# Performance work log

Measured on AMD Instinct MI355X. Metric: run time of the kernel, lower is better.

The kernel has to match this reference:

```python
import jax, jax.numpy as jnp
import numpy as np

NC = 80          # num classes
REG_MAX = 16     # DFL bins
STRIDES = (8, 16, 32)
FEAT_HW = ((80, 80), (40, 40), (20, 20))
MAX_DET = 100
CONF_THRES = 0.25
IOU_THRES = 0.45
PRE_TOPK = 1000  # pre-NMS candidate count (EfficientNMS-style preselection)


def setup_inputs() -> dict:
    key = jax.random.key(0)
    k1, k2, k3 = jax.random.split(key, 3)
    B = 32
    no = 4 * REG_MAX + NC  # 144
    return {
        "p3": jax.random.normal(k1, (B, no, 80, 80), dtype=jnp.float32),
        "p4": jax.random.normal(k2, (B, no, 40, 40), dtype=jnp.float32),
        "p5": jax.random.normal(k3, (B, no, 20, 20), dtype=jnp.float32),
    }


def _make_anchors():
    # grid_cell_offset = 0.5, matching ultralytics make_anchors
    pts, strs = [], []
    for (h, w), s in zip(FEAT_HW, STRIDES):
        sx = jnp.arange(w, dtype=jnp.float32) + 0.5
        sy = jnp.arange(h, dtype=jnp.float32) + 0.5
        yy, xx = jnp.meshgrid(sy, sx, indexing="ij")
        pts.append(jnp.stack([xx.ravel(), yy.ravel()], axis=-1))  # [h*w, 2]
        strs.append(jnp.full((h * w, 1), float(s), dtype=jnp.float32))
    return jnp.concatenate(pts, 0), jnp.concatenate(strs, 0)  # [A,2], [A,1]


def _pairwise_iou(b):
    # b: [K, 4] xyxy
    area = (b[:, 2] - b[:, 0]) * (b[:, 3] - b[:, 1])
    lt = jnp.maximum(b[:, None, :2], b[None, :, :2])
    rb = jnp.minimum(b[:, None, 2:], b[None, :, 2:])
    wh = jnp.clip(rb - lt, 0.0)
    inter = wh[..., 0] * wh[..., 1]
    return inter / (area[:, None] + area[None, :] - inter + 1e-7)


def _nms_single(bxyxy, conf):
    # Greedy class-agnostic NMS over PRE_TOPK score-sorted boxes.
    K = bxyxy.shape[0]
    iou = _pairwise_iou(bxyxy)  # [K, K]
    idx = jnp.arange(K)

    def step(suppressed, xs):
        i, row = xs
        keep = jnp.logical_and(jnp.logical_not(suppressed[i]), conf[i] > 0.0)
        suppressed = jnp.logical_or(suppressed, keep & (row > IOU_THRES) & (idx > i))
        return suppressed, keep

    _, keeps = jax.lax.scan(step, jnp.zeros(K, dtype=bool), (idx, iou))
    return keeps  # [K] bool


def reference(p3, p4, p5):
    feats = [p3, p4, p5]
    B = p3.shape[0]
    no = 4 * REG_MAX + NC
    # concat across scales: [B, no, A]
    x_cat = jnp.concatenate([f.reshape(B, no, -1) for f in feats], axis=2)
    box, cls = x_cat[:, : 4 * REG_MAX], x_cat[:, 4 * REG_MAX:]

    anchors, strd = _make_anchors()  # [A,2], [A,1]
    A = box.shape[-1]

    # DFL: softmax over reg_max bins, expectation with arange weights
    prob = jax.nn.softmax(box.reshape(B, 4, REG_MAX, A), axis=2)
    dist = jnp.einsum("bkra,r->bka", prob, jnp.arange(REG_MAX, dtype=jnp.float32))

    # dist2bbox (xywh) then scale by stride
    anc = anchors.T  # [2, A]
    lt, rb = dist[:, :2], dist[:, 2:]
    x1y1 = anc - lt
    x2y2 = anc + rb
    dbox = jnp.concatenate([(x1y1 + x2y2) * 0.5, x2y2 - x1y1], axis=1) * strd.T  # [B,4,A]

    boxes = dbox.transpose(0, 2, 1)                       # [B, A, 4] xywh
    scores = jax.nn.sigmoid(cls).transpose(0, 2, 1)       # [B, A, NC] (score_activation=1)

    # class-agnostic: best class per box
    conf = scores.max(-1)                                 # [B, A]
    cls_id = jnp.argmax(scores, -1)                       # [B, A]
    conf_m = jnp.where(conf > CONF_THRES, conf, -1.0)

    topv, topi = jax.lax.top_k(conf_m, PRE_TOPK)          # [B, K]
    bsel = jnp.take_along_axis(boxes, topi[..., None], axis=1)  # [B, K, 4]
    cx, cy, w, h = bsel[..., 0], bsel[..., 1], bsel[..., 2], bsel[..., 3]
    bxyxy = jnp.stack([cx - w * 0.5, cy - h * 0.5, cx + w * 0.5, cy + h * 0.5], -1)

    keeps = jax.vmap(_nms_single)(bxyxy, topv)            # [B, K]
    kept_scores = jnp.where(keeps, topv, -1.0)
    dv, di = jax.lax.top_k(kept_scores, MAX_DET)          # [B, MAX_DET]
    valid = dv > 0.0

    det_scores = jnp.where(valid, dv, 0.0)
    det_boxes = jnp.take_along_axis(bxyxy, di[..., None], axis=1) * valid[..., None]
    sel_cls = jnp.take_along_axis(jnp.take_along_axis(cls_id, topi, 1), di, 1)
    det_classes = jnp.where(valid, sel_cls, 0).astype(jnp.int32)
    num_dets = valid.sum(-1, keepdims=True).astype(jnp.int32)
    return num_dets, det_boxes, det_scores, det_classes
```

## Files before the change

kernel.cpp:

```cpp
#include <hip/hip_runtime.h>
#include <math.h>

#define NCLS 80
#define NA 8400
#define NB 32
#define NO 144
#define PRE_TOPK 1000
#define MAX_DET 100

template<int HW, int WDIM, int S>
__device__ __forceinline__ void decode_blk(
    const float* __restrict__ src, int b, int a0, int aoff,
    float* __restrict__ conf, int* __restrict__ clsid, float* __restrict__ box,
    float* s_tile)
{
    int t = threadIdx.x;
    int w = t >> 6;
    int l = t & 63;

    {
        int ch_base = w * 36;
        int chl = ch_base + (l >> 4);
        int aq = (l & 15) * 4;
        int aqc = a0 + aq; if (aqc > HW - 4) aqc = HW - 4;
        const float* gsrc = src + ((size_t)b * NO) * HW + aqc;
        float4 stg[9];
        #pragma unroll
        for (int i = 0; i < 9; ++i)
            stg[i] = *(const float4*)(gsrc + (size_t)(chl + i * 4) * HW);
        #pragma unroll
        for (int i = 0; i < 9; ++i)
            *(float4*)&s_tile[(chl + i * 4) * 64 + aq] = stg[i];
    }
    __syncthreads();

    float v[16];
    #pragma unroll
    for (int r = 0; r < 16; ++r) v[r] = s_tile[(w * 16 + r) * 64 + l];
    float mm = v[0];
    #pragma unroll
    for (int r = 1; r < 16; ++r) mm = fmaxf(mm, v[r]);
    float sum = 0.f, d = 0.f;
    #pragma unroll
    for (int r = 0; r < 16; ++r) {
        float e = __expf(v[r] - mm);
        sum += e;
        d += e * (float)r;
    }
    d *= 1.0f / sum;

    float c[20];
    #pragma unroll
    for (int cc = 0; cc < 20; ++cc) c[cc] = s_tile[(64 + w * 20 + cc) * 64 + l];
    float m = c[0]; int ii = 0;
    #pragma unroll
    for (int cc = 1; cc < 20; ++cc) if (c[cc] > m) { m = c[cc]; ii = cc; }

    __syncthreads();

    float* s_dfl = s_tile;
    float* s_mx  = s_tile + 320;
    int*   s_id  = (int*)(s_tile + 640);
    s_dfl[l * 5 + w] = d;
    s_mx[l * 5 + w]  = m;
    s_id[l * 5 + w]  = w * 20 + ii;
    __syncthreads();

    if (t < 64 && a0 + t < HW) {
        int pos2 = a0 + t;
        float d0 = s_dfl[t * 5 + 0], d1 = s_dfl[t * 5 + 1];
        float d2 = s_dfl[t * 5 + 2], d3 = s_dfl[t * 5 + 3];
        float bm = s_mx[t * 5 + 0]; int bid = s_id[t * 5 + 0];
        float m1 = s_mx[t * 5 + 1]; if (m1 > bm) { bm = m1; bid = s_id[t * 5 + 1]; }
        float m2 = s_mx[t * 5 + 2]; if (m2 > bm) { bm = m2; bid = s_id[t * 5 + 2]; }
        float m3 = s_mx[t * 5 + 3]; if (m3 > bm) { bm = m3; bid = s_id[t * 5 + 3]; }
        float conf_v = 1.0f / (1.0f + __expf(-bm));

        float ax = (float)(pos2 % WDIM) + 0.5f;
        float ay = (float)(pos2 / WDIM) + 0.5f;
        float x1 = ax - d0, y1 = ay - d1;
        float x2 = ax + d2, y2 = ay + d3;
        float cx = ((x1 + x2) * 0.5f) * (float)S;
        float cy = ((y1 + y2) * 0.5f) * (float)S;
        float ww = (x2 - x1) * (float)S;
        float hh = (y2 - y1) * (float)S;

        size_t gid = (size_t)b * NA + aoff + pos2;
        conf[gid]  = conf_v;
        clsid[gid] = bid;
        *(float4*)(box + gid * 4) = make_float4(cx, cy, ww, hh);
    }
}

__global__ __launch_bounds__(256) void k_decode(
    const float* __restrict__ p3, const float* __restrict__ p4, const float* __restrict__ p5,
    float* __restrict__ conf, int* __restrict__ clsid, float* __restrict__ box)
{
    __shared__ float s_tile[NO * 64];
    int blk = blockIdx.x;
    int b = blk / 132;
    int r = blk - b * 132;
    if (r < 100)       decode_blk<6400, 80, 8>(p3, b, r * 64, 0, conf, clsid, box, s_tile);
    else if (r < 125)  decode_blk<1600, 40, 16>(p4, b, (r - 100) * 64, 6400, conf, clsid, box, s_tile);
    else               decode_blk<400, 20, 32>(p5, b, (r - 125) * 64, 8000, conf, clsid, box, s_tile);
}

__device__ __forceinline__ uint32_t ord_bits(float f) {
    uint32_t u = __float_as_uint(f);
    return (u & 0x80000000u) ? ~u : (u | 0x80000000u);
}

__global__ __launch_bounds__(1024) void k_select(
    const float* __restrict__ conf, const float* __restrict__ box, const int* __restrict__ clsid,
    float* __restrict__ topv, float* __restrict__ bxyxy, int* __restrict__ topcls)
{
    int b = blockIdx.x;
    int t = threadIdx.x;
    int lane = t & 63;

    __shared__ uint32_t hist[256];
    __shared__ uint64_t sbuf[1024];
    __shared__ uint32_t s_prefix;
    __shared__ int s_k;
    __shared__ int s_cnt;

    const float* cf = conf + (size_t)b * NA;
    uint32_t kr[9];
    #pragma unroll
    for (int p = 0; p < 9; ++p) {
        int i = t + p * 1024;
        uint32_t k = 0;
        if (i < NA) {
            float c = cf[i];
            float cm = (c > 0.25f) ? c : -1.0f;
            k = ord_bits(cm);
        }
        kr[p] = k;
    }
    if (t == 0) { s_prefix = 0; s_k = PRE_TOPK; s_cnt = 0; }
    sbuf[t] = 0;
    __syncthreads();

    for (int pass = 0; pass < 4; ++pass) {
        int shift = 24 - 8 * pass;
        if (t < 256) hist[t] = 0;
        __syncthreads();
        uint32_t prefix = s_prefix;
        int k = s_k;
        #pragma unroll
        for (int p = 0; p < 9; ++p) {
            int i = t + p * 1024;
            uint32_t key = kr[p];
            bool match = (i < NA) &&
                         ((pass == 0) || (((key ^ prefix) >> (32 - 8 * pass)) == 0));
            uint32_t d = (key >> shift) & 255u;
            if (match) {
                uint64_t m = __ballot(1);
                #pragma unroll
                for (int bb = 0; bb < 8; ++bb) {
                    uint64_t bal = __ballot((d >> bb) & 1u);
                    m &= ((d >> bb) & 1u) ? bal : ~bal;
                }
                if ((m & ((1ull << lane) - 1ull)) == 0ull)
                    atomicAdd(&hist[d], (uint32_t)__popcll(m));
            }
        }
        __syncthreads();
        if (t < 64) {
            uint32_t h0 = hist[4 * t + 0], h1 = hist[4 * t + 1];
            uint32_t h2 = hist[4 * t + 2], h3 = hist[4 * t + 3];
            uint32_t part = h0 + h1 + h2 + h3;
            uint32_t s = part;
            #pragma unroll
            for (int off = 1; off < 64; off <<= 1) {
                uint32_t v = __shfl_down(s, off);
                if (t + off < 64) s += v;
            }
            uint32_t cb3 = s - part;
            uint32_t cb2 = cb3 + h3;
            uint32_t cb1 = cb2 + h2;
            uint32_t cb0 = cb1 + h1;
            uint32_t ku = (uint32_t)k;
            if (cb3 < ku && ku <= cb3 + h3) { s_k = k - (int)cb3; s_prefix = prefix | ((uint32_t)(4 * t + 3) << shift); }
            if (cb2 < ku && ku <= cb2 + h2) { s_k = k - (int)cb2; s_prefix = prefix | ((uint32_t)(4 * t + 2) << shift); }
            if (cb1 < ku && ku <= cb1 + h1) { s_k = k - (int)cb1; s_prefix = prefix | ((uint32_t)(4 * t + 1) << shift); }
            if (cb0 < ku && ku <= cb0 + h0) { s_k = k - (int)cb0; s_prefix = prefix | ((uint32_t)(4 * t + 0) << shift); }
        }
        __syncthreads();
    }

    uint32_t kstar = s_prefix;
    #pragma unroll
    for (int p = 0; p < 9; ++p) {
        int i = t + p * 1024;
        uint32_t key = kr[p];
        if (i < NA && key >= kstar) {
            int pos = atomicAdd(&s_cnt, 1);
            if (pos < 1024) sbuf[pos] = ((uint64_t)key << 14) | (uint64_t)(16383 - i);
        }
    }
    __syncthreads();

    uint64_t v = sbuf[t];
    for (int k = 2; k <= 1024; k <<= 1) {
        for (int j = k >> 1; j > 0; j >>= 1) {
            uint64_t o;
            if (j >= 64) {
                sbuf[t] = v;
                __syncthreads();
                o = sbuf[t ^ j];
                __syncthreads();
            } else {
                o = __shfl_xor((unsigned long long)v, j);
            }
            bool desc  = ((t & k) == 0);
            bool lower = ((t & j) == 0);
            v = (desc == lower) ? (v > o ? v : o) : (v < o ? v : o);
        }
    }

    if (t < PRE_TOPK) {
        uint64_t key = v;
        uint32_t u = (uint32_t)(key >> 14);
        uint32_t fb = (u & 0x80000000u) ? (u ^ 0x80000000u) : ~u;
        float val = __uint_as_float(fb);
        int idx = 16383 - (int)(key & 16383u);
        size_t g = (size_t)b * NA + idx;
        float4 bx = *(const float4*)(box + g * 4);
        float cx = bx.x, cy = bx.y, w = bx.z, h = bx.w;
        size_t o = (size_t)b * PRE_TOPK + t;
        topv[o] = val;
        *(float4*)(bxyxy + o * 4) = make_float4(cx - w * 0.5f, cy - h * 0.5f,
                                                cx + w * 0.5f, cy + h * 0.5f);
        topcls[o] = clsid[g];
    }
}

__device__ __forceinline__ int bslot(int j) { return j + (j >> 6); }

__global__ __launch_bounds__(256) void k_iou(
    const float* __restrict__ bxyxy, unsigned long long* __restrict__ mask)
{
    __shared__ float4 boxes[PRE_TOPK + 16];
    int b = blockIdx.y;
    int t = threadIdx.x;
    const float4* bp = (const float4*)(bxyxy + (size_t)b * PRE_TOPK * 4);
    for (int i = t; i < PRE_TOPK; i += 256) boxes[bslot(i)] = bp[i];
    __syncthreads();

    int r_local = t >> 4, w = t & 15;
    int row = blockIdx.x * 16 + r_local;
    if (row >= PRE_TOPK) return;

    float4 bi = boxes[bslot(row)];
    float area_i = (bi.z - bi.x) * (bi.w - bi.y);
    unsigned long long bits = 0;
    int j0 = w * 64;
    #pragma unroll 4
    for (int jj = 0; jj < 64; ++jj) {
        int j = j0 + jj;
        if (j >= PRE_TOPK) break;
        if (j <= row) continue;
        float4 bj = boxes[bslot(j)];
        float lx = fmaxf(bi.x, bj.x), ly = fmaxf(bi.y, bj.y);
        float rx = fminf(bi.z, bj.z), ry = fminf(bi.w, bj.w);
        float iw = fmaxf(rx - lx, 0.f), ih = fmaxf(ry - ly, 0.f);
        float inter = iw * ih;
        float area_j = (bj.z - bj.x) * (bj.w - bj.y);
        float iou = inter / (area_i + area_j - inter + 1e-7f);
        if (iou > 0.45f) bits |= (1ull << jj);
    }
    mask[((size_t)b * PRE_TOPK + row) * 16 + w] = bits;
}

__global__ __launch_bounds__(1024) void k_nms(
    const unsigned long long* __restrict__ mask, const float* __restrict__ topv,
    const float* __restrict__ bxyxy, const int* __restrict__ topcls,
    float* __restrict__ out)
{
    int b = blockIdx.x;
    int t = threadIdx.x;

    __shared__ __align__(16) unsigned long long smask[PRE_TOPK * 16];
    __shared__ float sv[PRE_TOPK];
    __shared__ unsigned long long s_valid[16];
    __shared__ int kept[MAX_DET];
    __shared__ int s_cnt;

    for (int i = t; i < PRE_TOPK; i += 1024) sv[i] = topv[(size_t)b * PRE_TOPK + i];
    {
        const ulonglong2* src = (const ulonglong2*)(mask + (size_t)b * PRE_TOPK * 16);
        ulonglong2* dst = (ulonglong2*)smask;
        for (int i = t; i < PRE_TOPK * 8; i += 1024) dst[i] = src[i];
    }
    __syncthreads();

    {
        bool pred = (t < PRE_TOPK) && (sv[t] > 0.0f);
        unsigned long long bal = __ballot(pred);
        if ((t & 63) == 0) s_valid[t >> 6] = bal;
    }
    __syncthreads();

    if (t < 64) {
        int w = t;
        unsigned long long supp = 0;
        unsigned long long valid = (w < 16) ? s_valid[w] : 0ull;
        int base = w * 64;
        int cur = -1;
        int cnt = 0;
        while (cnt < MAX_DET) {
            unsigned long long gt;
            if (cur < base)            gt = ~0ull;
            else if (cur - base >= 63) gt = 0ull;
            else                       gt = (~0ull) << (cur - base + 1);
            unsigned long long cand = valid & ~supp & gt;
            int idx = cand ? (base + __builtin_ctzll(cand)) : 0x7FFFFFFF;
            #pragma unroll
            for (int off = 8; off >= 1; off >>= 1) {
                int o = __shfl_xor(idx, off);
                idx = (o < idx) ? o : idx;
            }
            int nxt = __shfl(idx, 0);
            if (nxt == 0x7FFFFFFF) break;
            if (t == 0) kept[cnt] = nxt;
            ++cnt;
            if (w < 16) supp |= smask[nxt * 16 + w];
            cur = nxt;
        }
        if (t == 0) s_cnt = cnt;
    }
    __syncthreads();

    int cnt = s_cnt; if (cnt > MAX_DET) cnt = MAX_DET;
    if (t == 0) out[b] = (float)cnt;
    if (t < MAX_DET) {
        bool valid = t < cnt;
        float bx0 = 0.f, bx1 = 0.f, bx2 = 0.f, bx3 = 0.f, sc = 0.f, cl = 0.f;
        if (valid) {
            int p = kept[t];
            size_t o = (size_t)b * PRE_TOPK + p;
            float4 bb = *(const float4*)(bxyxy + o * 4);
            bx0 = bb.x; bx1 = bb.y; bx2 = bb.z; bx3 = bb.w;
            sc = sv[p];
            cl = (float)topcls[o];
        }
        size_t db = 32 + ((size_t)b * MAX_DET + t) * 4;
        out[db + 0] = bx0; out[db + 1] = bx1; out[db + 2] = bx2; out[db + 3] = bx3;
        out[32 + 12800 + (size_t)b * MAX_DET + t] = sc;
        out[32 + 16000 + (size_t)b * MAX_DET + t] = cl;
    }
}

extern "C" void kernel_launch(void* const* d_in, const int* in_sizes, int n_in,
                              void* d_out, int out_size, void* d_ws, size_t ws_size,
                              hipStream_t stream)
{
    const float* p3 = (const float*)d_in[0];
    const float* p4 = (const float*)d_in[1];
    const float* p5 = (const float*)d_in[2];
    float* out = (float*)d_out;

    char* ws = (char*)d_ws;
    size_t off_mask = 0;
    size_t off_conf = off_mask + (size_t)NB * PRE_TOPK * 16 * 8;
    size_t off_cls  = off_conf + (size_t)NB * NA * 4;
    size_t off_box  = off_cls  + (size_t)NB * NA * 4;
    size_t off_topv = off_box  + (size_t)NB * NA * 4 * 4;
    size_t off_topc = off_topv + (size_t)NB * PRE_TOPK * 4;
    size_t off_bx   = off_topc + (size_t)NB * PRE_TOPK * 4;

    unsigned long long* mask = (unsigned long long*)(ws + off_mask);
    float* conf   = (float*)(ws + off_conf);
    int*   clsid  = (int*)(ws + off_cls);
    float* box    = (float*)(ws + off_box);
    float* topv   = (float*)(ws + off_topv);
    int*   topcls = (int*)(ws + off_topc);
    float* bxyxy  = (float*)(ws + off_bx);

    k_decode<<<NB * 132, 256, 0, stream>>>(p3, p4, p5, conf, clsid, box);
    k_select<<<NB, 1024, 0, stream>>>(conf, box, clsid, topv, bxyxy, topcls);
    k_iou<<<dim3((PRE_TOPK + 15) / 16, NB), 256, 0, stream>>>(bxyxy, mask);
    k_nms<<<NB, 1024, 0, stream>>>(mask, topv, bxyxy, topcls, out);
}
```

Measured before the change: 132.5 us.

## Defer DFL box decoding to top-K survivors in select kernel

```diff
diff --git a/kernel.cpp b/kernel.cpp
--- a/kernel.cpp
+++ b/kernel.cpp
@@ -8,101 +8,68 @@
 #define PRE_TOPK 1000
 #define MAX_DET 100
 
-template<int HW, int WDIM, int S>
-__device__ __forceinline__ void decode_blk(
+template<int HW, int WDIM>
+__device__ __forceinline__ void decode_cls_blk(
     const float* __restrict__ src, int b, int a0, int aoff,
-    float* __restrict__ conf, int* __restrict__ clsid, float* __restrict__ box,
-    float* s_tile)
+    float* __restrict__ conf, int* __restrict__ clsid, float* s_tile)
 {
     int t = threadIdx.x;
     int w = t >> 6;
     int l = t & 63;
 
     {
-        int ch_base = w * 36;
-        int chl = ch_base + (l >> 4);
+        int chl = w * 20 + (l >> 4);
         int aq = (l & 15) * 4;
         int aqc = a0 + aq; if (aqc > HW - 4) aqc = HW - 4;
-        const float* gsrc = src + ((size_t)b * NO) * HW + aqc;
-        float4 stg[9];
-        #pragma unroll
-        for (int i = 0; i < 9; ++i)
+        const float* gsrc = src + ((size_t)b * NO + 64) * HW + aqc;
+        float4 stg[5];
+        #pragma unroll
+        for (int i = 0; i < 5; ++i)
             stg[i] = *(const float4*)(gsrc + (size_t)(chl + i * 4) * HW);
         #pragma unroll
-        for (int i = 0; i < 9; ++i)
+        for (int i = 0; i < 5; ++i)
             *(float4*)&s_tile[(chl + i * 4) * 64 + aq] = stg[i];
     }
     __syncthreads();
 
-    float v[16];
-    #pragma unroll
-    for (int r = 0; r < 16; ++r) v[r] = s_tile[(w * 16 + r) * 64 + l];
-    float mm = v[0];
-    #pragma unroll
-    for (int r = 1; r < 16; ++r) mm = fmaxf(mm, v[r]);
-    float sum = 0.f, d = 0.f;
-    #pragma unroll
-    for (int r = 0; r < 16; ++r) {
-        float e = __expf(v[r] - mm);
-        sum += e;
-        d += e * (float)r;
-    }
-    d *= 1.0f / sum;
-
     float c[20];
     #pragma unroll
-    for (int cc = 0; cc < 20; ++cc) c[cc] = s_tile[(64 + w * 20 + cc) * 64 + l];
+    for (int cc = 0; cc < 20; ++cc) c[cc] = s_tile[(w * 20 + cc) * 64 + l];
     float m = c[0]; int ii = 0;
     #pragma unroll
     for (int cc = 1; cc < 20; ++cc) if (c[cc] > m) { m = c[cc]; ii = cc; }
 
     __syncthreads();
 
-    float* s_dfl = s_tile;
-    float* s_mx  = s_tile + 320;
-    int*   s_id  = (int*)(s_tile + 640);
-    s_dfl[l * 5 + w] = d;
-    s_mx[l * 5 + w]  = m;
-    s_id[l * 5 + w]  = w * 20 + ii;
+    float* s_mx = s_tile;
+    int*   s_id = (int*)(s_tile + 320);
+    s_mx[l * 5 + w] = m;
+    s_id[l * 5 + w] = w * 20 + ii;
     __syncthreads();
 
     if (t < 64 && a0 + t < HW) {
-        int pos2 = a0 + t;
-        float d0 = s_dfl[t * 5 + 0], d1 = s_dfl[t * 5 + 1];
-        float d2 = s_dfl[t * 5 + 2], d3 = s_dfl[t * 5 + 3];
         float bm = s_mx[t * 5 + 0]; int bid = s_id[t * 5 + 0];
         float m1 = s_mx[t * 5 + 1]; if (m1 > bm) { bm = m1; bid = s_id[t * 5 + 1]; }
         float m2 = s_mx[t * 5 + 2]; if (m2 > bm) { bm = m2; bid = s_id[t * 5 + 2]; }
         float m3 = s_mx[t * 5 + 3]; if (m3 > bm) { bm = m3; bid = s_id[t * 5 + 3]; }
         float conf_v = 1.0f / (1.0f + __expf(-bm));
-
-        float ax = (float)(pos2 % WDIM) + 0.5f;
-        float ay = (float)(pos2 / WDIM) + 0.5f;
-        float x1 = ax - d0, y1 = ay - d1;
-        float x2 = ax + d2, y2 = ay + d3;
-        float cx = ((x1 + x2) * 0.5f) * (float)S;
-        float cy = ((y1 + y2) * 0.5f) * (float)S;
-        float ww = (x2 - x1) * (float)S;
-        float hh = (y2 - y1) * (float)S;
-
-        size_t gid = (size_t)b * NA + aoff + pos2;
+        size_t gid = (size_t)b * NA + aoff + (a0 + t);
         conf[gid]  = conf_v;
         clsid[gid] = bid;
-        *(float4*)(box + gid * 4) = make_float4(cx, cy, ww, hh);
     }
 }
 
 __global__ __launch_bounds__(256) void k_decode(
     const float* __restrict__ p3, const float* __restrict__ p4, const float* __restrict__ p5,
-    float* __restrict__ conf, int* __restrict__ clsid, float* __restrict__ box)
-{
-    __shared__ float s_tile[NO * 64];
+    float* __restrict__ conf, int* __restrict__ clsid)
+{
+    __shared__ float s_tile[80 * 64];
     int blk = blockIdx.x;
     int b = blk / 132;
     int r = blk - b * 132;
-    if (r < 100)       decode_blk<6400, 80, 8>(p3, b, r * 64, 0, conf, clsid, box, s_tile);
-    else if (r < 125)  decode_blk<1600, 40, 16>(p4, b, (r - 100) * 64, 6400, conf, clsid, box, s_tile);
-    else               decode_blk<400, 20, 32>(p5, b, (r - 125) * 64, 8000, conf, clsid, box, s_tile);
+    if (r < 100)       decode_cls_blk<6400, 80>(p3, b, r * 64, 0, conf, clsid, s_tile);
+    else if (r < 125)  decode_cls_blk<1600, 40>(p4, b, (r - 100) * 64, 6400, conf, clsid, s_tile);
+    else               decode_cls_blk<400, 20>(p5, b, (r - 125) * 64, 8000, conf, clsid, s_tile);
 }
 
 __device__ __forceinline__ uint32_t ord_bits(float f) {
@@ -110,8 +77,41 @@
     return (u & 0x80000000u) ? ~u : (u | 0x80000000u);
 }
 
+__device__ __forceinline__ float4 dfl_box(const float* __restrict__ base,
+                                          int HW, int pos, int WDIM, float S)
+{
+    float dist[4];
+    #pragma unroll
+    for (int s4 = 0; s4 < 4; ++s4) {
+        float v[16];
+        #pragma unroll
+        for (int r = 0; r < 16; ++r) v[r] = base[(size_t)(s4 * 16 + r) * HW];
+        float mm = v[0];
+        #pragma unroll
+        for (int r = 1; r < 16; ++r) mm = fmaxf(mm, v[r]);
+        float sum = 0.f, d = 0.f;
+        #pragma unroll
+        for (int r = 0; r < 16; ++r) {
+            float e = __expf(v[r] - mm);
+            sum += e;
+            d += e * (float)r;
+        }
+        dist[s4] = d * (1.0f / sum);
+    }
+    float ax = (float)(pos % WDIM) + 0.5f;
+    float ay = (float)(pos / WDIM) + 0.5f;
+    float x1 = ax - dist[0], y1 = ay - dist[1];
+    float x2 = ax + dist[2], y2 = ay + dist[3];
+    float cx = ((x1 + x2) * 0.5f) * S;
+    float cy = ((y1 + y2) * 0.5f) * S;
+    float w  = (x2 - x1) * S;
+    float h  = (y2 - y1) * S;
+    return make_float4(cx - w * 0.5f, cy - h * 0.5f, cx + w * 0.5f, cy + h * 0.5f);
+}
+
 __global__ __launch_bounds__(1024) void k_select(
-    const float* __restrict__ conf, const float* __restrict__ box, const int* __restrict__ clsid,
+    const float* __restrict__ conf, const int* __restrict__ clsid,
+    const float* __restrict__ p3, const float* __restrict__ p4, const float* __restrict__ p5,
     float* __restrict__ topv, float* __restrict__ bxyxy, int* __restrict__ topcls)
 {
     int b = blockIdx.x;
@@ -225,14 +225,25 @@
         uint32_t fb = (u & 0x80000000u) ? (u ^ 0x80000000u) : ~u;
         float val = __uint_as_float(fb);
         int idx = 16383 - (int)(key & 16383u);
-        size_t g = (size_t)b * NA + idx;
-        float4 bx = *(const float4*)(box + g * 4);
-        float cx = bx.x, cy = bx.y, w = bx.z, h = bx.w;
+
+        float4 bb;
+        if (idx < 6400) {
+            const float* base = p3 + ((size_t)b * NO) * 6400 + idx;
+            bb = dfl_box(base, 6400, idx, 80, 8.f);
+        } else if (idx < 8000) {
+            int pos = idx - 6400;
+            const float* base = p4 + ((size_t)b * NO) * 1600 + pos;
+            bb = dfl_box(base, 1600, pos, 40, 16.f);
+        } else {
+            int pos = idx - 8000;
+            const float* base = p5 + ((size_t)b * NO) * 400 + pos;
+            bb = dfl_box(base, 400, pos, 20, 32.f);
+        }
+
         size_t o = (size_t)b * PRE_TOPK + t;
         topv[o] = val;
-        *(float4*)(bxyxy + o * 4) = make_float4(cx - w * 0.5f, cy - h * 0.5f,
-                                                cx + w * 0.5f, cy + h * 0.5f);
-        topcls[o] = clsid[g];
+        *(float4*)(bxyxy + o * 4) = bb;
+        topcls[o] = clsid[(size_t)b * NA + idx];
     }
 }
 
@@ -365,21 +376,19 @@
     size_t off_mask = 0;
     size_t off_conf = off_mask + (size_t)NB * PRE_TOPK * 16 * 8;
     size_t off_cls  = off_conf + (size_t)NB * NA * 4;
-    size_t off_box  = off_cls  + (size_t)NB * NA * 4;
-    size_t off_topv = off_box  + (size_t)NB * NA * 4 * 4;
+    size_t off_topv = off_cls  + (size_t)NB * NA * 4;
     size_t off_topc = off_topv + (size_t)NB * PRE_TOPK * 4;
     size_t off_bx   = off_topc + (size_t)NB * PRE_TOPK * 4;
 
     unsigned long long* mask = (unsigned long long*)(ws + off_mask);
     float* conf   = (float*)(ws + off_conf);
     int*   clsid  = (int*)(ws + off_cls);
-    float* box    = (float*)(ws + off_box);
     float* topv   = (float*)(ws + off_topv);
     int*   topcls = (int*)(ws + off_topc);
     float* bxyxy  = (float*)(ws + off_bx);
 
-    k_decode<<<NB * 132, 256, 0, stream>>>(p3, p4, p5, conf, clsid, box);
-    k_select<<<NB, 1024, 0, stream>>>(conf, box, clsid, topv, bxyxy, topcls);
+    k_decode<<<NB * 132, 256, 0, stream>>>(p3, p4, p5, conf, clsid);
+    k_select<<<NB, 1024, 0, stream>>>(conf, clsid, p3, p4, p5, topv, bxyxy, topcls);
     k_iou<<<dim3((PRE_TOPK + 15) / 16, NB), 256, 0, stream>>>(bxyxy, mask);
     k_nms<<<NB, 1024, 0, stream>>>(mask, topv, bxyxy, topcls, out);
 }
```

New measurement: 189.5 us. 43.1% more time.
